# Optimization experiments

Hardware: AMD Instinct MI355X
Metric: run time of the kernel (lower is better)

Reference implementation:

```python
import jax, jax.numpy as jnp
import numpy as np

B, N, D = 4, 1024, 1024
H = 16
DH = D // H  # 64
DROPOUT_P = 0.5


def setup_inputs() -> dict:
    key = jax.random.key(0)
    ks = jax.random.split(key, 6)
    query = jax.random.normal(ks[0], (B, N, D), dtype=jnp.float32)
    key_t = jax.random.normal(ks[1], (B, N, D), dtype=jnp.float32)
    value = jax.random.normal(ks[2], (B, N, D), dtype=jnp.float32)
    # torch Linear(D, 3D): weight [3D, D], bias [3D]
    W_qkv = jax.random.normal(ks[3], (3 * D, D), dtype=jnp.float32) * (1.0 / np.sqrt(D))
    b_qkv = jax.random.normal(ks[4], (3 * D,), dtype=jnp.float32) * 0.01
    # inverted dropout mask: keep_prob = 1 - p, kept entries scaled by 1/keep
    keep = 1.0 - DROPOUT_P
    drop_mask = (jax.random.uniform(ks[5], (B * H, N, N)) < keep).astype(jnp.float32) / keep
    return {"query": query, "key": key_t, "value": value,
            "W_qkv": W_qkv, "b_qkv": b_qkv, "drop_mask": drop_mask}


def _split_heads(t):
    # 'b n (h d) -> (b h) n d'
    b, n, _ = t.shape
    return t.reshape(b, n, H, DH).transpose(0, 2, 1, 3).reshape(b * H, n, DH)


def reference(query, key, value, W_qkv, b_qkv, drop_mask):
    # key/value args are unused by the original module (it derives q,k,v from query)
    qkv = query @ W_qkv.T + b_qkv                      # [b, n, 3d]
    q, k, v = jnp.split(qkv, 3, axis=-1)
    q, k, v = _split_heads(q), _split_heads(k), _split_heads(v)  # [(b h), n, dh]
    qk = jnp.einsum('znd,zmd->znm', q, k)              # [(b h), n, n]
    # faithful quirk: original does qk.div(1/sqrt(dh)) == qk * sqrt(dh)
    scaled_qk = qk * jnp.sqrt(jnp.float32(DH))
    attn = jax.nn.softmax(scaled_qk, axis=-1)
    attn = attn * drop_mask                            # deterministic inverted dropout
    out = jnp.einsum('znm,zmd->znd', attn, v)          # [(b h), n, dh]
    # '(b h) n d -> b n (h d)'
    out = out.reshape(B, H, N, DH).transpose(0, 2, 1, 3).reshape(B, N, D)
    return out
```

## Files before the change

kernel.cpp:

```cpp
#include <hip/hip_runtime.h>


typedef _Float16 f16;
typedef _Float16 f16x4 __attribute__((ext_vector_type(4)));
typedef _Float16 f16x8 __attribute__((ext_vector_type(8)));
typedef float    f32x4 __attribute__((ext_vector_type(4)));
typedef unsigned long long u64;

#define MFMA16(a, b, c) __builtin_amdgcn_mfma_f32_16x16x32_f16((a), (b), (c), 0, 0, 0)

__device__ __forceinline__ void gll16(const f16* g, f16* l) {
  __builtin_amdgcn_global_load_lds(
      (const __attribute__((address_space(1))) unsigned int*)g,
      (__attribute__((address_space(3))) unsigned int*)l, 16, 0, 0);
}

__device__ __forceinline__ f16x8 ldsfrag(const f16* tile, int row, int chunk) {
  return *(const f16x8*)&tile[row * 64 + ((chunk ^ (row & 7)) << 3)];
}

__global__ __launch_bounds__(256) void cvt_split(const float4* __restrict__ s,
                                                 f16x4* __restrict__ hi,
                                                 f16x4* __restrict__ lo, int n4) {
  int i = blockIdx.x * 256 + threadIdx.x;
  if (i >= n4) return;
  float4 v = s[i];
  f16x4 h, l;
  h[0] = (f16)v.x; l[0] = (f16)(v.x - (float)h[0]);
  h[1] = (f16)v.y; l[1] = (f16)(v.y - (float)h[1]);
  h[2] = (f16)v.z; l[2] = (f16)(v.z - (float)h[2]);
  h[3] = (f16)v.w; l[3] = (f16)(v.w - (float)h[3]);
  hi[i] = h; lo[i] = l;
}

__global__ __launch_bounds__(256) void mask_bits(const float* __restrict__ mask,
                                                 u64* __restrict__ bits) {
  const int gw = (blockIdx.x * 256 + threadIdx.x) >> 6;
  const int lane = threadIdx.x & 63;
  for (int r = gw; r < 65536; r += 4096) {
    const float* mrow = mask + (size_t)r * 1024;
    u64* brow = bits + (size_t)r * 16;
#pragma unroll
    for (int kw = 0; kw < 16; ++kw) {
      float v = mrow[kw * 64 + lane];
      u64 b = __ballot(v > 1.0f);
      if (lane == 0) brow[kw] = b;
    }
  }
}

__global__ __launch_bounds__(256) void proj_gemm(
    const f16* __restrict__ qh, const f16* __restrict__ ql,
    const f16* __restrict__ wh, const f16* __restrict__ wl,
    const float* __restrict__ bias,
    f16* __restrict__ Qh, f16* __restrict__ Ql,
    f16* __restrict__ Kh, f16* __restrict__ Kl,
    f16* __restrict__ Vh) {
  __shared__ f16 Ah[128 * 32], Al[128 * 32], Bh[128 * 32], Bl[128 * 32];
  const int tid = threadIdx.x;
  const int bid = blockIdx.x;
  const int wg = (bid & 7) * 96 + (bid >> 3);
  const int m0 = (wg / 24) * 128, n0 = (wg % 24) * 128;
  const bool isv = (n0 >= 2048);
  const int wid = tid >> 6, lane = tid & 63;
  const int wm = (wid >> 1) * 64, wn = (wid & 1) * 64;
  const int r16 = lane & 15, g = lane >> 4;

  f32x4 zero4 = {0.f, 0.f, 0.f, 0.f};
  f32x4 acc[4][4];
#pragma unroll
  for (int i = 0; i < 4; ++i)
#pragma unroll
    for (int j = 0; j < 4; ++j) acc[i][j] = zero4;

  for (int s = 0; s < 32; ++s) {
    const int kk = s << 5;
    const f16* Abh = qh + (size_t)m0 * 1024 + kk;
    const f16* Abl = ql + (size_t)m0 * 1024 + kk;
    const f16* Bbh = wh + (size_t)n0 * 1024 + kk;
    const f16* Bbl = wl + (size_t)n0 * 1024 + kk;
#pragma unroll
    for (int it = 0; it < 2; ++it) {
      const int c = tid + it * 256;
      const int go = (c >> 2) * 1024 + (c & 3) * 8;
      gll16(Abh + go, &Ah[c * 8]);
      gll16(Bbh + go, &Bh[c * 8]);
      if (!isv) {
        gll16(Abl + go, &Al[c * 8]);
        gll16(Bbl + go, &Bl[c * 8]);
      }
    }
    __syncthreads();
    f16x8 a[4], al_[4];
#pragma unroll
    for (int i = 0; i < 4; ++i) {
      a[i] = *(const f16x8*)&Ah[(wm + i * 16 + r16) * 32 + g * 8];
      if (!isv) al_[i] = *(const f16x8*)&Al[(wm + i * 16 + r16) * 32 + g * 8];
    }
#pragma unroll
    for (int j = 0; j < 4; ++j) {
      const f16x8 b = *(const f16x8*)&Bh[(wn + j * 16 + r16) * 32 + g * 8];
      if (!isv) {
        const f16x8 bl = *(const f16x8*)&Bl[(wn + j * 16 + r16) * 32 + g * 8];
#pragma unroll
        for (int i = 0; i < 4; ++i) {
          acc[i][j] = MFMA16(a[i], b, acc[i][j]);
          acc[i][j] = MFMA16(al_[i], b, acc[i][j]);
          acc[i][j] = MFMA16(a[i], bl, acc[i][j]);
        }
      } else {
#pragma unroll
        for (int i = 0; i < 4; ++i) acc[i][j] = MFMA16(a[i], b, acc[i][j]);
      }
    }
    __syncthreads();
  }

#pragma unroll
  for (int j = 0; j < 4; ++j) {
    const int col = n0 + wn + j * 16 + r16;
    const float bv = bias[col];
#pragma unroll
    for (int i = 0; i < 4; ++i) {
#pragma unroll
      for (int rr = 0; rr < 4; ++rr) {
        const int m = m0 + wm + i * 16 + g * 4 + rr;
        const float c = acc[i][j][rr] + bv;
        const int bi = m >> 10, n = m & 1023;
        if (col < 1024) {
          const int z = bi * 16 + (col >> 6), dh = col & 63;
          const size_t idx = ((size_t)z * 1024 + n) * 64 + dh;
          f16 h = (f16)c;
          Qh[idx] = h; Ql[idx] = (f16)(c - (float)h);
        } else if (col < 2048) {
          const int c2 = col - 1024;
          const int z = bi * 16 + (c2 >> 6), dh = c2 & 63;
          const size_t idx = ((size_t)z * 1024 + n) * 64 + dh;
          f16 h = (f16)c;
          Kh[idx] = h; Kl[idx] = (f16)(c - (float)h);
        } else {
          const int c2 = col - 2048;
          const int z = bi * 16 + (c2 >> 6), dh = c2 & 63;
          Vh[((size_t)z * 1024 + n) * 64 + dh] = (f16)c;
        }
      }
    }
  }
}

__global__ __launch_bounds__(256) void transp_v(const f16* __restrict__ Vh,
                                                f16* __restrict__ Vt) {
  __shared__ f16 t[64][80];
  const int z = blockIdx.y, nt = blockIdx.x;
  const int tid = threadIdx.x;
#pragma unroll
  for (int it = 0; it < 2; ++it) {
    int c = tid + it * 256;
    int row = c >> 3, cc = c & 7;
    *(f16x8*)&t[row][cc * 8] =
        *(const f16x8*)&Vh[(((size_t)z << 10) + nt * 64 + row) * 64 + cc * 8];
  }
  __syncthreads();
#pragma unroll
  for (int it = 0; it < 2; ++it) {
    int c = tid + it * 256;
    int dh = c >> 3, ncc = c & 7;
    f16x8 o;
#pragma unroll
    for (int j = 0; j < 8; ++j) o[j] = t[ncc * 8 + j][dh];
    *(f16x8*)&Vt[((size_t)z * 64 + dh) * 1024 + nt * 64 + ncc * 8] = o;
  }
}

__global__ __launch_bounds__(512) void attn(
    const f16* __restrict__ Qh_, const f16* __restrict__ Ql_,
    const f16* __restrict__ Kh_, const f16* __restrict__ Kl_,
    const f16* __restrict__ Vt_, const u64* __restrict__ bits,
    float* __restrict__ out) {
  __shared__ f16 Khs[2][4096], Kls[2][4096], Vts[2][4096];
  __shared__ f16 Ps[8][1024];

  const int bid = blockIdx.x;
  const int wg = (bid & 7) * 64 + (bid >> 3);
  const int qt = wg & 7, z = wg >> 3;
  const int q0 = qt * 128;
  const int tid = threadIdx.x, w = tid >> 6, lane = tid & 63;
  const int r16 = lane & 15, g = lane >> 4;

  const size_t zrow = (size_t)z << 10;
  const f16* qrh = Qh_ + (zrow + q0 + w * 16 + r16) * 64;
  const f16* qrl = Ql_ + (zrow + q0 + w * 16 + r16) * 64;
  f16x8 qa[2], qla[2];
#pragma unroll
  for (int ks = 0; ks < 2; ++ks) {
    qa[ks] = *(const f16x8*)&qrh[ks * 32 + g * 8];
    qla[ks] = *(const f16x8*)&qrl[ks * 32 + g * 8];
  }

  const f16* KzhB = Kh_ + zrow * 64;
  const f16* KzlB = Kl_ + zrow * 64;
  const f16* VzB = Vt_ + (size_t)z * 64 * 1024;
  const int sc = tid, srow = sc >> 3, ssc = ((sc & 7) ^ (srow & 7)) << 3;

#define STAGE(buf, k0_)                                                   \
  do {                                                                    \
    gll16(KzhB + (size_t)((k0_) + srow) * 64 + ssc, &Khs[buf][sc * 8]);   \
    gll16(KzlB + (size_t)((k0_) + srow) * 64 + ssc, &Kls[buf][sc * 8]);   \
    gll16(VzB + (size_t)srow * 1024 + (k0_) + ssc, &Vts[buf][sc * 8]);    \
  } while (0)

  STAGE(0, 0);

  float mrow[4] = {-1e30f, -1e30f, -1e30f, -1e30f};
  float lrow[4] = {0.f, 0.f, 0.f, 0.f};
  f32x4 zero4 = {0.f, 0.f, 0.f, 0.f};
  f32x4 acc[4];
#pragma unroll
  for (int df = 0; df < 4; ++df) acc[df] = zero4;

  const int qrow_m = q0 + w * 16 + g * 4;
  const u64* brow = bits + (zrow + qrow_m) * 16;
  f16* Pw = &Ps[w][0];
  __syncthreads();

  for (int kt = 0; kt < 16; ++kt) {
    const int cur = kt & 1;
    const int k0 = kt << 6;
    if (kt < 15) STAGE(cur ^ 1, k0 + 64);

    u64 bm[4];
#pragma unroll
    for (int rr = 0; rr < 4; ++rr) bm[rr] = brow[rr * 16 + kt];

    __builtin_amdgcn_s_setprio(1);
    f32x4 s[4];
#pragma unroll
    for (int cf = 0; cf < 4; ++cf) {
      const int krow = cf * 16 + r16;
      const f16x8 kh0 = ldsfrag(&Khs[cur][0], krow, g);
      const f16x8 kh1 = ldsfrag(&Khs[cur][0], krow, 4 + g);
      const f16x8 kl0 = ldsfrag(&Kls[cur][0], krow, g);
      const f16x8 kl1 = ldsfrag(&Kls[cur][0], krow, 4 + g);
      f32x4 t = zero4;
      t = MFMA16(qa[0], kh0, t);
      t = MFMA16(qla[0], kh0, t);
      t = MFMA16(qa[0], kl0, t);
      t = MFMA16(qa[1], kh1, t);
      t = MFMA16(qla[1], kh1, t);
      t = MFMA16(qa[1], kl1, t);
      s[cf] = t;
    }
    __builtin_amdgcn_s_setprio(0);

    float s8[4][4];
#pragma unroll
    for (int cf = 0; cf < 4; ++cf)
#pragma unroll
      for (int rr = 0; rr < 4; ++rr) s8[cf][rr] = s[cf][rr] * 8.0f;

    float rm[4];
#pragma unroll
    for (int rr = 0; rr < 4; ++rr)
      rm[rr] = fmaxf(fmaxf(s8[0][rr], s8[1][rr]), fmaxf(s8[2][rr], s8[3][rr]));
#pragma unroll
    for (int mk = 1; mk < 16; mk <<= 1)
#pragma unroll
      for (int rr = 0; rr < 4; ++rr)
        rm[rr] = fmaxf(rm[rr], __shfl_xor(rm[rr], mk, 64));

    const int nogrow = __all((rm[0] <= mrow[0] + 8.f) & (rm[1] <= mrow[1] + 8.f) &
                             (rm[2] <= mrow[2] + 8.f) & (rm[3] <= mrow[3] + 8.f));
    if (!nogrow) {
      float scal[4];
#pragma unroll
      for (int rr = 0; rr < 4; ++rr) {
        const float mnew = fmaxf(mrow[rr], rm[rr]);
        scal[rr] = __expf(mrow[rr] - mnew);
        mrow[rr] = mnew;
        lrow[rr] *= scal[rr];
      }
#pragma unroll
      for (int df = 0; df < 4; ++df)
#pragma unroll
        for (int rr = 0; rr < 4; ++rr) acc[df][rr] *= scal[rr];
    }

    float p_[4][4], rs[4] = {0.f, 0.f, 0.f, 0.f};
#pragma unroll
    for (int cf = 0; cf < 4; ++cf)
#pragma unroll
      for (int rr = 0; rr < 4; ++rr) {
        p_[cf][rr] = __expf(s8[cf][rr] - mrow[rr]);
        rs[rr] += p_[cf][rr];
      }
#pragma unroll
    for (int mk = 1; mk < 16; mk <<= 1)
#pragma unroll
      for (int rr = 0; rr < 4; ++rr) rs[rr] += __shfl_xor(rs[rr], mk, 64);
#pragma unroll
    for (int rr = 0; rr < 4; ++rr) lrow[rr] += rs[rr];

#pragma unroll
    for (int cf = 0; cf < 4; ++cf)
#pragma unroll
      for (int rr = 0; rr < 4; ++rr) {
        const int prow = g * 4 + rr, key = cf * 16 + r16;
        const float pm =
            ((bm[rr] >> key) & 1ull) ? p_[cf][rr] + p_[cf][rr] : 0.0f;
        Pw[prow * 64 + (((key >> 3) ^ (prow & 7)) << 3) + (key & 7)] = (f16)pm;
      }
    f16x8 pf[2];
#pragma unroll
    for (int ks2 = 0; ks2 < 2; ++ks2)
      pf[ks2] = ldsfrag(Pw, r16, ks2 * 4 + g);

    __builtin_amdgcn_s_setprio(1);
#pragma unroll
    for (int df = 0; df < 4; ++df)
#pragma unroll
      for (int ks2 = 0; ks2 < 2; ++ks2)
        acc[df] = MFMA16(pf[ks2],
                         ldsfrag(&Vts[cur][0], df * 16 + r16, ks2 * 4 + g),
                         acc[df]);
    __builtin_amdgcn_s_setprio(0);
    __syncthreads();
  }

  const int bi = z >> 4, hh = z & 15;
#pragma unroll
  for (int df = 0; df < 4; ++df)
#pragma unroll
    for (int rr = 0; rr < 4; ++rr) {
      const int n = q0 + w * 16 + g * 4 + rr;
      out[((size_t)bi * 1024 + n) * 1024 + hh * 64 + df * 16 + r16] =
          acc[df][rr] / lrow[rr];
    }
#undef STAGE
}

extern "C" void kernel_launch(void* const* d_in, const int* in_sizes, int n_in,
                              void* d_out, int out_size, void* d_ws,
                              size_t ws_size, hipStream_t stream) {
  const float* query = (const float*)d_in[0];
  const float* W = (const float*)d_in[3];
  const float* bias = (const float*)d_in[4];
  const float* mask = (const float*)d_in[5];
  float* out = (float*)d_out;

  f16* p = (f16*)d_ws;
  f16* qh = p;              p += (size_t)4096 * 1024;
  f16* ql = p;              p += (size_t)4096 * 1024;
  f16* wh = p;              p += (size_t)3072 * 1024;
  f16* wl = p;              p += (size_t)3072 * 1024;
  f16* Qh = p;              p += (size_t)64 * 1024 * 64;
  f16* Ql = p;              p += (size_t)64 * 1024 * 64;
  f16* Kh = p;              p += (size_t)64 * 1024 * 64;
  f16* Kl = p;              p += (size_t)64 * 1024 * 64;
  f16* Vh = p;              p += (size_t)64 * 1024 * 64;
  f16* Vt = p;              p += (size_t)64 * 1024 * 64;
  u64* bits = (u64*)p;

  mask_bits<<<1024, 256, 0, stream>>>(mask, bits);
  cvt_split<<<(1048576 + 255) / 256, 256, 0, stream>>>(
      (const float4*)query, (f16x4*)qh, (f16x4*)ql, 1048576);
  cvt_split<<<(786432 + 255) / 256, 256, 0, stream>>>(
      (const float4*)W, (f16x4*)wh, (f16x4*)wl, 786432);
  proj_gemm<<<768, 256, 0, stream>>>(qh, ql, wh, wl, bias, Qh, Ql, Kh, Kl, Vh);
  transp_v<<<dim3(16, 64), 256, 0, stream>>>(Vh, Vt);
  attn<<<512, 512, 0, stream>>>(Qh, Ql, Kh, Kl, Vt, bits, out);
}
```

Measured before the change: 661.8 us.

## Double-buffer projection GEMM LDS tiles and vectorize mask bit packing

The projection GEMM now uses two LDS buffers and issues the async global-to-LDS loads for the next K slice before computing the current one, so load latency overlaps MFMA work and one barrier per iteration is dropped. The mask-packing kernel is rewritten so each thread reads four float4s and writes a 16-bit packed mask word directly, replacing the per-wave ballot loop with a fully parallel launch. Double buffering doubles LDS use per block, which may lower occupancy. The packed bit order must match what the attention kernel expects when it reads the mask as u64 words.

```diff
diff --git a/kernel.cpp b/kernel.cpp
--- a/kernel.cpp
+++ b/kernel.cpp
@@ -6,6 +6,7 @@
 typedef _Float16 f16x8 __attribute__((ext_vector_type(8)));
 typedef float    f32x4 __attribute__((ext_vector_type(4)));
 typedef unsigned long long u64;
+typedef unsigned short u16;
 
 #define MFMA16(a, b, c) __builtin_amdgcn_mfma_f32_16x16x32_f16((a), (b), (c), 0, 0, 0)
 
@@ -33,20 +34,23 @@
   hi[i] = h; lo[i] = l;
 }
 
-__global__ __launch_bounds__(256) void mask_bits(const float* __restrict__ mask,
-                                                 u64* __restrict__ bits) {
-  const int gw = (blockIdx.x * 256 + threadIdx.x) >> 6;
-  const int lane = threadIdx.x & 63;
-  for (int r = gw; r < 65536; r += 4096) {
-    const float* mrow = mask + (size_t)r * 1024;
-    u64* brow = bits + (size_t)r * 16;
-#pragma unroll
-    for (int kw = 0; kw < 16; ++kw) {
-      float v = mrow[kw * 64 + lane];
-      u64 b = __ballot(v > 1.0f);
-      if (lane == 0) brow[kw] = b;
-    }
-  }
+__global__ __launch_bounds__(256) void mask_bits(const float4* __restrict__ mask,
+                                                 u16* __restrict__ bits16) {
+  const size_t t = (size_t)blockIdx.x * 256 + threadIdx.x;
+  const float4 v0 = mask[t * 4 + 0];
+  const float4 v1 = mask[t * 4 + 1];
+  const float4 v2 = mask[t * 4 + 2];
+  const float4 v3 = mask[t * 4 + 3];
+  unsigned m = 0;
+  m |= (v0.x > 1.f) ? 0x0001u : 0u;  m |= (v0.y > 1.f) ? 0x0002u : 0u;
+  m |= (v0.z > 1.f) ? 0x0004u : 0u;  m |= (v0.w > 1.f) ? 0x0008u : 0u;
+  m |= (v1.x > 1.f) ? 0x0010u : 0u;  m |= (v1.y > 1.f) ? 0x0020u : 0u;
+  m |= (v1.z > 1.f) ? 0x0040u : 0u;  m |= (v1.w > 1.f) ? 0x0080u : 0u;
+  m |= (v2.x > 1.f) ? 0x0100u : 0u;  m |= (v2.y > 1.f) ? 0x0200u : 0u;
+  m |= (v2.z > 1.f) ? 0x0400u : 0u;  m |= (v2.w > 1.f) ? 0x0800u : 0u;
+  m |= (v3.x > 1.f) ? 0x1000u : 0u;  m |= (v3.y > 1.f) ? 0x2000u : 0u;
+  m |= (v3.z > 1.f) ? 0x4000u : 0u;  m |= (v3.w > 1.f) ? 0x8000u : 0u;
+  bits16[t] = (u16)m;
 }
 
 __global__ __launch_bounds__(256) void proj_gemm(
@@ -56,7 +60,8 @@
     f16* __restrict__ Qh, f16* __restrict__ Ql,
     f16* __restrict__ Kh, f16* __restrict__ Kl,
     f16* __restrict__ Vh) {
-  __shared__ f16 Ah[128 * 32], Al[128 * 32], Bh[128 * 32], Bl[128 * 32];
+  __shared__ f16 Ah[2][128 * 32], Al[2][128 * 32];
+  __shared__ f16 Bh[2][128 * 32], Bl[2][128 * 32];
   const int tid = threadIdx.x;
   const int bid = blockIdx.x;
   const int wg = (bid & 7) * 96 + (bid >> 3);
@@ -66,6 +71,28 @@
   const int wm = (wid >> 1) * 64, wn = (wid & 1) * 64;
   const int r16 = lane & 15, g = lane >> 4;
 
+  const int c0 = tid, c1 = tid + 256;
+  const int go0 = (c0 >> 2) * 1024 + (c0 & 3) * 8;
+  const int go1 = (c1 >> 2) * 1024 + (c1 & 3) * 8;
+  const f16* Aqh = qh + (size_t)m0 * 1024;
+  const f16* Aql = ql + (size_t)m0 * 1024;
+  const f16* Bwh = wh + (size_t)n0 * 1024;
+  const f16* Bwl = wl + (size_t)n0 * 1024;
+
+#define PSTAGE(buf, kk_)                                  \
+  do {                                                    \
+    gll16(Aqh + (kk_) + go0, &Ah[buf][c0 * 8]);           \
+    gll16(Aqh + (kk_) + go1, &Ah[buf][c1 * 8]);           \
+    gll16(Bwh + (kk_) + go0, &Bh[buf][c0 * 8]);           \
+    gll16(Bwh + (kk_) + go1, &Bh[buf][c1 * 8]);           \
+    if (!isv) {                                           \
+      gll16(Aql + (kk_) + go0, &Al[buf][c0 * 8]);         \
+      gll16(Aql + (kk_) + go1, &Al[buf][c1 * 8]);         \
+      gll16(Bwl + (kk_) + go0, &Bl[buf][c0 * 8]);         \
+      gll16(Bwl + (kk_) + go1, &Bl[buf][c1 * 8]);         \
+    }                                                     \
+  } while (0)
+
   f32x4 zero4 = {0.f, 0.f, 0.f, 0.f};
   f32x4 acc[4][4];
 #pragma unroll
@@ -73,35 +100,26 @@
 #pragma unroll
     for (int j = 0; j < 4; ++j) acc[i][j] = zero4;
 
+  PSTAGE(0, 0);
+  __syncthreads();
+
   for (int s = 0; s < 32; ++s) {
-    const int kk = s << 5;
-    const f16* Abh = qh + (size_t)m0 * 1024 + kk;
-    const f16* Abl = ql + (size_t)m0 * 1024 + kk;
-    const f16* Bbh = wh + (size_t)n0 * 1024 + kk;
-    const f16* Bbl = wl + (size_t)n0 * 1024 + kk;
-#pragma unroll
-    for (int it = 0; it < 2; ++it) {
-      const int c = tid + it * 256;
-      const int go = (c >> 2) * 1024 + (c & 3) * 8;
-      gll16(Abh + go, &Ah[c * 8]);
-      gll16(Bbh + go, &Bh[c * 8]);
+    const int cur = s & 1;
+    if (s < 31) PSTAGE(cur ^ 1, (s + 1) << 5);
+
+    f16x8 a[4], al_[4];
+#pragma unroll
+    for (int i = 0; i < 4; ++i) {
+      a[i] = *(const f16x8*)&Ah[cur][(wm + i * 16 + r16) * 32 + g * 8];
+      if (!isv)
+        al_[i] = *(const f16x8*)&Al[cur][(wm + i * 16 + r16) * 32 + g * 8];
+    }
+#pragma unroll
+    for (int j = 0; j < 4; ++j) {
+      const f16x8 b = *(const f16x8*)&Bh[cur][(wn + j * 16 + r16) * 32 + g * 8];
       if (!isv) {
-        gll16(Abl + go, &Al[c * 8]);
-        gll16(Bbl + go, &Bl[c * 8]);
-      }
-    }
-    __syncthreads();
-    f16x8 a[4], al_[4];
-#pragma unroll
-    for (int i = 0; i < 4; ++i) {
-      a[i] = *(const f16x8*)&Ah[(wm + i * 16 + r16) * 32 + g * 8];
-      if (!isv) al_[i] = *(const f16x8*)&Al[(wm + i * 16 + r16) * 32 + g * 8];
-    }
-#pragma unroll
-    for (int j = 0; j < 4; ++j) {
-      const f16x8 b = *(const f16x8*)&Bh[(wn + j * 16 + r16) * 32 + g * 8];
-      if (!isv) {
-        const f16x8 bl = *(const f16x8*)&Bl[(wn + j * 16 + r16) * 32 + g * 8];
+        const f16x8 bl =
+            *(const f16x8*)&Bl[cur][(wn + j * 16 + r16) * 32 + g * 8];
 #pragma unroll
         for (int i = 0; i < 4; ++i) {
           acc[i][j] = MFMA16(a[i], b, acc[i][j]);
@@ -115,6 +133,7 @@
     }
     __syncthreads();
   }
+#undef PSTAGE
 
 #pragma unroll
   for (int j = 0; j < 4; ++j) {
@@ -360,7 +379,7 @@
   f16* Vt = p;              p += (size_t)64 * 1024 * 64;
   u64* bits = (u64*)p;
 
-  mask_bits<<<1024, 256, 0, stream>>>(mask, bits);
+  mask_bits<<<16384, 256, 0, stream>>>((const float4*)mask, (u16*)bits);
   cvt_split<<<(1048576 + 255) / 256, 256, 0, stream>>>(
       (const float4*)query, (f16x4*)qh, (f16x4*)ql, 1048576);
   cvt_split<<<(786432 + 255) / 256, 256, 0, stream>>>(
```

Result: faster. 573.9 us (-13.3%).
